# Optimization experiments

Measured on AMD Instinct MI355X. Metric: run time of the kernel, lower is better.

Reference implementation:

```python
import jax, jax.numpy as jnp
import numpy as np

B, L, D = 4, 4096, 1024
N_HEADS = 16
HEAD_SIZE = D // N_HEADS  # 64


def setup_inputs() -> dict:
    key = jax.random.key(0)
    k_x, k_w, k_m = jax.random.split(key, 3)
    x = jax.random.normal(k_x, (B, L, D), dtype=jnp.float32)
    # nn.Linear(D, 3*head_size, bias=False): weight (3*hs, D); store transposed (D, 3*hs)
    W_qkv = jax.random.normal(k_w, (D, 3 * HEAD_SIZE), dtype=jnp.float32) * (D ** -0.5)
    attn_mask = jax.random.randint(k_m, (B, L), 0, 2).astype(jnp.bool_)
    return {"x": x, "attn_mask": attn_mask, "W_qkv": W_qkv}


def reference(x, attn_mask, W_qkv):
    # x: (B, L, D); W_qkv: (D, 3*hs); attn_mask: (B, L) True = attend
    qkv = x @ W_qkv                                # (B, L, 3*hs)
    q, k, v = jnp.split(qkv, 3, axis=-1)           # each (B, L, hs)
    scale = HEAD_SIZE ** -0.5
    scores = jnp.einsum('bqd,bkd->bqk', q, k) * scale   # (B, L, L)
    neg_inf = jnp.finfo(scores.dtype).min
    scores = jnp.where(attn_mask[:, None, :], scores, neg_inf)
    weights = jax.nn.softmax(scores, axis=-1)      # (B, L, L)
    out = jnp.einsum('bqk,bkd->bqd', weights, v)   # (B, L, hs)
    return out
```

## Files before the change

kernel.cpp:

```cpp
#include <hip/hip_runtime.h>

typedef __bf16 bf16_t;
typedef __bf16 bf16x8 __attribute__((ext_vector_type(8)));
typedef __bf16 bf16x4 __attribute__((ext_vector_type(4)));
typedef __bf16 bf16x2 __attribute__((ext_vector_type(2)));
typedef float  f32x4  __attribute__((ext_vector_type(4)));
typedef float  f32x16 __attribute__((ext_vector_type(16)));
struct uint4_t { unsigned x, y, z, w; };

#define B_  4
#define L_  4096
#define D_  1024
#define HS  64
#define NQ  192
#define SCL2E 0.1803368801111204f
#define MFMA16 __builtin_amdgcn_mfma_f32_16x16x32_bf16
#define MFMA32 __builtin_amdgcn_mfma_f32_32x32x16_bf16

#if defined(__has_builtin)
# if __has_builtin(__builtin_amdgcn_global_load_lds)
#  define HAS_GLL 1
# endif
#endif
#ifndef HAS_GLL
# define HAS_GLL 0
#endif

static __device__ __forceinline__ unsigned pk_bf16(float a, float b) {
    union { bf16x2 v; unsigned u; } x;
    x.v[0] = (bf16_t)a; x.v[1] = (bf16_t)b;
    return x.u;
}
static __device__ __forceinline__ void swap32(unsigned& x, unsigned& y) {
    asm("v_permlane32_swap_b32 %0, %1" : "+v"(x), "+v"(y));
}

__global__ __launch_bounds__(256) void pack_w_kernel(const void* __restrict__ Win,
                                                     const unsigned char* __restrict__ mask,
                                                     const unsigned short* __restrict__ xw,
                                                     bf16_t* __restrict__ Wtp,
                                                     int* __restrict__ flags,
                                                     bf16_t* __restrict__ m01) {
    __shared__ int c1, c23, cbad;
    int tid = threadIdx.x;
    if (tid == 0) { c1 = 0; c23 = 0; cbad = 0; }
    __syncthreads();
    uint4_t m[4];
#pragma unroll
    for (int i = 0; i < 4; ++i)
        m[i] = *(const uint4_t*)(mask + tid * 16 + i * 4096);
    int a = 0, bc = 0;
#pragma unroll
    for (int i = 0; i < 4; ++i) {
        const unsigned* w = (const unsigned*)&m[i];
#pragma unroll
        for (int j = 0; j < 4; ++j) {
            if (w[j] & 0x0000ff00u) a++;
            if (w[j] & 0xffff0000u) bc++;
        }
    }
    uint4_t xm = *(const uint4_t*)(xw + tid * 8);
    int bad = 0;
    const unsigned* xwv = (const unsigned*)&xm;
#pragma unroll
    for (int j = 0; j < 4; ++j)
#pragma unroll
        for (int h = 0; h < 2; ++h) {
            unsigned s = (xwv[j] >> (16 * h)) & 0xFFFFu;
            unsigned e = (s >> 7) & 0xFF;
            if (e > 150 || (e < 90 && e != 0)) bad++;
        }
    if (a)   atomicAdd(&c1, a);
    if (bc)  atomicAdd(&c23, bc);
    if (bad) atomicAdd(&cbad, bad);
    __syncthreads();
    int f32 = (cbad >= 64) ? 1 : 0;
    int kind = (c1 > 0) ? 1 : ((c23 > 0) ? 2 : 0);
    if (blockIdx.x == 0 && tid == 0) {
        flags[0] = kind;
        flags[1] = f32;
    }

    int idx = blockIdx.x * 256 + tid;

    if (idx < B_ * L_) {
        bool mv;
        if (kind == 1)      mv = mask[idx] != 0;
        else if (kind == 2) mv = ((const float*)mask)[idx] != 0.0f;
        else                mv = ((const int*)mask)[idx] != 0;
        m01[idx] = (bf16_t)(mv ? 1.0f : 0.0f);
    }

    int lane = idx & 63;
    int t    = (idx >> 6) & 3;
    int kc   = (idx >> 8) & 31;
    int ct   = idx >> 13;
    int n  = ct * 64 + t * 16 + (lane & 15);
    int k0 = kc * 32 + (lane >> 4) * 8;
    bf16x8 v;
#pragma unroll
    for (int j = 0; j < 8; ++j) {
        if (f32) v[j] = (bf16_t)(((const float*)Win)[(k0 + j) * NQ + n]);
        else     v[j] = ((const bf16_t*)Win)[(k0 + j) * NQ + n];
    }
    *(bf16x8*)(Wtp + (size_t)idx * 8) = v;
}

__global__ __launch_bounds__(256, 2) void qkv_gemm_kernel(const void* __restrict__ xin,
                                                          const int* __restrict__ flags,
                                                          const bf16_t* __restrict__ Wtp,
                                                          const bf16_t* __restrict__ m01p,
                                                          bf16_t* __restrict__ Qb,
                                                          bf16_t* __restrict__ Kp,
                                                          bf16_t* __restrict__ Vp) {
    __shared__ __align__(16) bf16_t xs[32 * 520];
    __shared__ __align__(16) bf16_t sqk[32 * 136];
    __shared__ __align__(16) bf16_t sv[64 * 40];

    int tid = threadIdx.x;
    int wave = tid >> 6, lane = tid & 63, quad = lane >> 4, l16 = lane & 15;
    int rg = wave & 1, ch = wave >> 1;
    int m0 = blockIdx.x * 32;
    int xf = flags[1];

    f32x4 acc[6] = {};
    bf16x8 Ba[6], Bb[6];

    auto stage = [&](int h) {
        bf16x8 tmp[8];
#pragma unroll
        for (int j = 0; j < 8; ++j) {
            int c = tid + j * 256;
            int row = c >> 6, off = (c & 63) * 8;
            if (xf) {
                const float* xp = (const float*)xin + (size_t)(m0 + row) * D_ + h * 512 + off;
                f32x4 lo = *(const f32x4*)xp, hi = *(const f32x4*)(xp + 4);
                tmp[j][0] = (bf16_t)lo[0]; tmp[j][1] = (bf16_t)lo[1];
                tmp[j][2] = (bf16_t)lo[2]; tmp[j][3] = (bf16_t)lo[3];
                tmp[j][4] = (bf16_t)hi[0]; tmp[j][5] = (bf16_t)hi[1];
                tmp[j][6] = (bf16_t)hi[2]; tmp[j][7] = (bf16_t)hi[3];
            } else {
                tmp[j] = *(const bf16x8*)((const bf16_t*)xin + (size_t)(m0 + row) * D_ + h * 512 + off);
            }
        }
#pragma unroll
        for (int j = 0; j < 8; ++j) {
            int c = tid + j * 256;
            int row = c >> 6, off = (c & 63) * 8;
            *(bf16x8*)&xs[row * 520 + off] = tmp[j];
        }
    };
    auto loadB6 = [&](int ks, bf16x8* Bv) {
#pragma unroll
        for (int i = 0; i < 6; ++i) {
            int st = ch * 6 + i, ct2 = st >> 2, tt = st & 3;
            Bv[i] = *(const bf16x8*)(Wtp + ((size_t)(ct2 * 32 + ks) * 4 + tt) * 512 + lane * 8);
        }
    };
    auto compute6 = [&](int ks, const bf16x8* Bv) {
        bf16x8 A = *(const bf16x8*)&xs[(rg * 16 + l16) * 520 + (ks & 15) * 32 + quad * 8];
#pragma unroll
        for (int i = 0; i < 6; ++i)
            acc[i] = MFMA16(A, Bv[i], acc[i], 0, 0, 0);
    };

    stage(0);
    loadB6(0, Ba);
    __syncthreads();
#pragma unroll
    for (int half = 0; half < 2; ++half) {
        int base = half * 16;
        for (int m = 0; m < 16; m += 2) {
            int ks = base + m;
            loadB6(ks + 1, Bb);
            compute6(ks, Ba);
            loadB6(ks + 2 <= 31 ? ks + 2 : 31, Ba);
            compute6(ks + 1, Bb);
        }
        if (half == 0) {
            __syncthreads();
            stage(1);
            __syncthreads();
        }
    }

    int rowb = rg * 16 + quad * 4;
#pragma unroll
    for (int i = 0; i < 6; ++i) {
        int col = ch * 96 + i * 16 + l16;
#pragma unroll
        for (int r = 0; r < 4; ++r) {
            float av = acc[i][r];
            if (col < 64) av *= SCL2E;
            bf16_t hv = (bf16_t)av;
            if (col < 128) sqk[(rowb + r) * 136 + col] = hv;
            else           sv[(col - 128) * 40 + rowb + r] = hv;
        }
    }
    __syncthreads();

    int bb = m0 >> 12, l0 = m0 & 4095;
    int t64 = l0 >> 6, stile = (l0 >> 5) & 1, ctop = (l0 >> 4) & 2;
    {
        int row = tid >> 3, off = (tid & 7) * 8;
        bf16x8 v = *(const bf16x8*)&sqk[row * 136 + off];
        *(bf16x8*)(Qb + (size_t)(m0 + row) * HS + off) = v;
    }
    {
        int chk = tid >> 6, ln = tid & 63;
        bf16x8 v = *(const bf16x8*)&sqk[(tid & 31) * 136 + 64 + chk * 16 + ((tid >> 5) & 1) * 8];
        *(bf16x8*)(Kp + (size_t)bb * (L_ * HS) +
                   ((((size_t)t64 * 2 + stile) * 4 + chk) * 64 + ln) * 8) = v;
    }
    {
        int dt = tid >> 7, chL = (tid >> 6) & 1, ln = tid & 63;
        int hi2 = (tid >> 5) & 1, d31 = tid & 31;
        bf16x8 v  = *(const bf16x8*)&sv[(dt * 32 + d31) * 40 + chL * 16 + hi2 * 8];
        bf16x8 mm = *(const bf16x8*)(m01p + (size_t)m0 + chL * 16 + hi2 * 8);
        bf16x8 o;
#pragma unroll
        for (int j = 0; j < 8; ++j) o[j] = (bf16_t)((float)v[j] * (float)mm[j]);
        *(bf16x8*)(Vp + (size_t)bb * (L_ * HS) +
                   ((((size_t)t64 * 2 + dt) * 4 + ctop + chL) * 64 + ln) * 8) = o;
    }
}

template<int NSPLIT>
__global__ __launch_bounds__(256, 2) void attn_kernel(const bf16_t* __restrict__ Qb,
                                                      const bf16_t* __restrict__ Kp,
                                                      const bf16_t* __restrict__ Vp,
                                                      const bf16_t* __restrict__ m01p,
                                                      const int* __restrict__ flags,
                                                      float* __restrict__ Opart,
                                                      float* __restrict__ lpart,
                                                      void* __restrict__ outv) {
    constexpr int KCH = L_ / NSPLIT;
    constexpr int NHT = KCH / 32;
    __shared__ __align__(16) bf16_t ktile[4][2][2048];

    int tid = threadIdx.x, wave = tid >> 6, lane = tid & 63;
    int hi = lane >> 5, l31 = lane & 31;
    int grp = blockIdx.x % (B_ * NSPLIT);
    int qt  = blockIdx.x / (B_ * NSPLIT);
    int sp = grp / B_, b = grp % B_;
    int q0 = qt * 128 + wave * 32;
    int hb = sp * NHT;

    const bf16_t* KpB = Kp + (size_t)b * (L_ * HS);
    const bf16_t* VpB = Vp + (size_t)b * (L_ * HS);
    const bf16_t* mB  = m01p + (size_t)b * L_ + sp * KCH;

    bf16x8 Qf[4];
    {
        const bf16_t* qp = Qb + (size_t)(b * L_ + q0 + l31) * HS + hi * 8;
#pragma unroll
        for (int c = 0; c < 4; ++c) Qf[c] = *(const bf16x8*)(qp + c * 16);
    }

    f32x16 O0 = {}, O1 = {}, den = {};

    auto stage = [&](int buf, int ht) {
        const bf16_t* src = KpB + (size_t)ht * 2048;
        bf16_t* dst = &ktile[wave][buf][0];
#if HAS_GLL
#pragma unroll
        for (int j = 0; j < 4; ++j)
            __builtin_amdgcn_global_load_lds(
                (const __attribute__((address_space(1))) unsigned*)(src + (j * 64 + lane) * 8),
                (__attribute__((address_space(3))) unsigned*)(dst + (j * 64 + lane) * 8), 16, 0, 0);
#else
#pragma unroll
        for (int j = 0; j < 4; ++j)
            *(bf16x8*)(dst + (j * 64 + lane) * 8) = *(const bf16x8*)(src + (j * 64 + lane) * 8);
#endif
    };

    stage(0, hb);
    if (NHT > 1) stage(1, hb + 1);

    for (int t = 0; t < NHT; ++t) {
        int ht = hb + t;
        int t64 = ht >> 1, stile = ht & 1;
        const bf16_t* vt = VpB + (size_t)t64 * 4096;
        const bf16_t* mt = mB + t * 32;

        bf16x8 V0[2], V1[2], Mf[2];
#pragma unroll
        for (int cc = 0; cc < 2; ++cc) {
            int chk = stile * 2 + cc;
            V0[cc] = *(const bf16x8*)(vt + (size_t)(0 * 4 + chk) * 512 + lane * 8);
            V1[cc] = *(const bf16x8*)(vt + (size_t)(1 * 4 + chk) * 512 + lane * 8);
            Mf[cc] = *(const bf16x8*)(mt + cc * 16 + hi * 8);
        }

        if (t + 1 < NHT) { asm volatile("s_waitcnt vmcnt(10)" ::: "memory"); }
        else             { asm volatile("s_waitcnt vmcnt(6)"  ::: "memory"); }

        const bf16_t* kl = &ktile[wave][t & 1][0];
        bf16x8 Kfr[4];
#pragma unroll
        for (int c = 0; c < 4; ++c)
            Kfr[c] = *(const bf16x8*)(kl + c * 512 + lane * 8);
        asm volatile("s_waitcnt lgkmcnt(0)" ::: "memory");
        __builtin_amdgcn_sched_barrier(0);
        if (t + 2 < NHT) stage(t & 1, ht + 2);

        f32x16 S = {};
        __builtin_amdgcn_s_setprio(1);
#pragma unroll
        for (int c = 0; c < 4; ++c)
            S = MFMA32(Kfr[c], Qf[c], S, 0, 0, 0);
        __builtin_amdgcn_s_setprio(0);
#pragma unroll
        for (int r = 0; r < 16; ++r) S[r] = exp2f(S[r]);

#pragma unroll
        for (int cc = 0; cc < 2; ++cc) {
            unsigned w0 = pk_bf16(S[cc * 8 + 0], S[cc * 8 + 1]);
            unsigned w1 = pk_bf16(S[cc * 8 + 2], S[cc * 8 + 3]);
            unsigned w2 = pk_bf16(S[cc * 8 + 4], S[cc * 8 + 5]);
            unsigned w3 = pk_bf16(S[cc * 8 + 6], S[cc * 8 + 7]);
            swap32(w0, w2);
            swap32(w1, w3);
            union { unsigned u[4]; bf16x8 v; } P;
            P.u[0] = w0; P.u[1] = w1; P.u[2] = w2; P.u[3] = w3;
            __builtin_amdgcn_s_setprio(1);
            O0  = MFMA32(P.v, V0[cc], O0, 0, 0, 0);
            O1  = MFMA32(P.v, V1[cc], O1, 0, 0, 0);
            den = MFMA32(P.v, Mf[cc], den, 0, 0, 0);
            __builtin_amdgcn_s_setprio(0);
        }
    }

    if (NSPLIT == 1) {
        int of32 = flags[1];
#pragma unroll
        for (int r = 0; r < 16; ++r) {
            int qr = (r & 3) + 8 * (r >> 2) + 4 * hi;
            float inv = 1.0f / den[r];
            size_t base = (size_t)(b * L_ + q0 + qr) * HS;
            if (of32) {
                float* op = (float*)outv + base;
                op[l31]      = O0[r] * inv;
                op[32 + l31] = O1[r] * inv;
            } else {
                bf16_t* op = (bf16_t*)outv + base;
                op[l31]      = (bf16_t)(O0[r] * inv);
                op[32 + l31] = (bf16_t)(O1[r] * inv);
            }
        }
    } else {
        float* op = Opart + (size_t)sp * (B_ * L_ * HS) + (size_t)(b * L_ + q0) * HS + l31;
#pragma unroll
        for (int r = 0; r < 16; ++r) {
            int qr = (r & 3) + 8 * (r >> 2) + 4 * hi;
            op[(size_t)qr * HS]      = O0[r];
            op[(size_t)qr * HS + 32] = O1[r];
        }
        if (l31 == 0) {
            float* lp = lpart + (size_t)sp * (B_ * L_) + b * L_ + q0;
#pragma unroll
            for (int r = 0; r < 16; ++r)
                lp[(r & 3) + 8 * (r >> 2) + 4 * hi] = den[r];
        }
    }
}

__global__ __launch_bounds__(256) void reduce_kernel(const float* __restrict__ Opart,
                                                     const float* __restrict__ lpart,
                                                     const int* __restrict__ flags,
                                                     void* __restrict__ outv,
                                                     int nsplit) {
    int i4 = (blockIdx.x * 256 + threadIdx.x) * 4;
    int row = i4 >> 6;
    f32x4 acc = {};
    float lsum = 0.f;
    for (int s = 0; s < nsplit; ++s) {
        acc  += *(const f32x4*)&Opart[(size_t)s * (B_ * L_ * HS) + i4];
        lsum += lpart[(size_t)s * (B_ * L_) + row];
    }
    float inv = 1.0f / lsum;
    if (flags[1]) {
        f32x4 r = { acc[0] * inv, acc[1] * inv, acc[2] * inv, acc[3] * inv };
        *(f32x4*)&((float*)outv)[i4] = r;
    } else {
        bf16x4 r;
#pragma unroll
        for (int j = 0; j < 4; ++j) r[j] = (bf16_t)(acc[j] * inv);
        *(bf16x4*)&((bf16_t*)outv)[i4] = r;
    }
}

extern "C" void kernel_launch(void* const* d_in, const int* in_sizes, int n_in,
                              void* d_out, int out_size, void* d_ws, size_t ws_size,
                              hipStream_t stream) {
    (void)in_sizes; (void)n_in; (void)out_size;
    const void* x    = d_in[0];
    const void* mask = d_in[1];
    const void* W    = d_in[2];

    char* ws = (char*)d_ws;
    bf16_t* Qb    = (bf16_t*)(ws);
    bf16_t* Kp    = (bf16_t*)(ws + (2u << 20));
    bf16_t* Vp    = (bf16_t*)(ws + (4u << 20));
    bf16_t* Wtp   = (bf16_t*)(ws + (6u << 20));
    int*    flags = (int*)   (ws + (6u << 20) + (512u << 10));
    bf16_t* m01p  = (bf16_t*)(ws + (6u << 20) + (516u << 10));
    float*  Opart = (float*) (ws + (7u << 20));

    auto need = [](int ns) -> size_t {
        return (7u << 20) + (size_t)ns * (B_ * L_ * HS * 4)
                          + (size_t)ns * (B_ * L_ * 4) + 4096;
    };
    int nsplit = (ws_size >= need(8)) ? 8 : (ws_size >= need(4)) ? 4 : 1;
    float* lpart = (float*)(ws + (7u << 20) + (size_t)nsplit * (B_ * L_ * HS * 4));

    pack_w_kernel<<<96, 256, 0, stream>>>(W, (const unsigned char*)mask,
                                          (const unsigned short*)x, Wtp, flags, m01p);
    qkv_gemm_kernel<<<512, 256, 0, stream>>>(x, flags, Wtp, m01p, Qb, Kp, Vp);
    if (nsplit == 8) {
        attn_kernel<8><<<32 * B_ * 8, 256, 0, stream>>>(Qb, Kp, Vp, m01p, flags,
                                                        Opart, lpart, d_out);
        reduce_kernel<<<(B_ * L_ * HS) / 1024, 256, 0, stream>>>(Opart, lpart, flags,
                                                                 d_out, 8);
    } else if (nsplit == 4) {
        attn_kernel<4><<<32 * B_ * 4, 256, 0, stream>>>(Qb, Kp, Vp, m01p, flags,
                                                        Opart, lpart, d_out);
        reduce_kernel<<<(B_ * L_ * HS) / 1024, 256, 0, stream>>>(Opart, lpart, flags,
                                                                 d_out, 4);
    } else {
        attn_kernel<1><<<32 * B_, 256, 0, stream>>>(Qb, Kp, Vp, m01p, flags,
                                                    Opart, lpart, d_out);
    }
}
```

Before: 164.3 us.

## Load K fragments directly from global and raise key-split count to 16

Drops the per-wave LDS double-buffered staging of K tiles (global_load_lds plus waitcnt choreography) and has each lane read its K fragments straight from global memory into registers. It also raises the key-dimension split from 8 to 16 when the workspace allows, launching twice as many attention blocks and reducing over 16 partials. The aim is to remove LDS traffic and sync overhead and to expose more parallelism. The cost is that K-load latency is no longer prefetched two tiles ahead, and the partial-output writes and reduction work grow.

```diff
diff --git a/kernel.cpp b/kernel.cpp
--- a/kernel.cpp
+++ b/kernel.cpp
@@ -16,15 +16,6 @@
 #define SCL2E 0.1803368801111204f
 #define MFMA16 __builtin_amdgcn_mfma_f32_16x16x32_bf16
 #define MFMA32 __builtin_amdgcn_mfma_f32_32x32x16_bf16
-
-#if defined(__has_builtin)
-# if __has_builtin(__builtin_amdgcn_global_load_lds)
-#  define HAS_GLL 1
-# endif
-#endif
-#ifndef HAS_GLL
-# define HAS_GLL 0
-#endif
 
 static __device__ __forceinline__ unsigned pk_bf16(float a, float b) {
     union { bf16x2 v; unsigned u; } x;
@@ -236,7 +227,6 @@
                                                       void* __restrict__ outv) {
     constexpr int KCH = L_ / NSPLIT;
     constexpr int NHT = KCH / 32;
-    __shared__ __align__(16) bf16_t ktile[4][2][2048];
 
     int tid = threadIdx.x, wave = tid >> 6, lane = tid & 63;
     int hi = lane >> 5, l31 = lane & 31;
@@ -259,31 +249,17 @@
 
     f32x16 O0 = {}, O1 = {}, den = {};
 
-    auto stage = [&](int buf, int ht) {
-        const bf16_t* src = KpB + (size_t)ht * 2048;
-        bf16_t* dst = &ktile[wave][buf][0];
-#if HAS_GLL
-#pragma unroll
-        for (int j = 0; j < 4; ++j)
-            __builtin_amdgcn_global_load_lds(
-                (const __attribute__((address_space(1))) unsigned*)(src + (j * 64 + lane) * 8),
-                (__attribute__((address_space(3))) unsigned*)(dst + (j * 64 + lane) * 8), 16, 0, 0);
-#else
-#pragma unroll
-        for (int j = 0; j < 4; ++j)
-            *(bf16x8*)(dst + (j * 64 + lane) * 8) = *(const bf16x8*)(src + (j * 64 + lane) * 8);
-#endif
-    };
-
-    stage(0, hb);
-    if (NHT > 1) stage(1, hb + 1);
-
     for (int t = 0; t < NHT; ++t) {
         int ht = hb + t;
         int t64 = ht >> 1, stile = ht & 1;
+        const bf16_t* kt = KpB + (size_t)ht * 2048;
         const bf16_t* vt = VpB + (size_t)t64 * 4096;
         const bf16_t* mt = mB + t * 32;
 
+        bf16x8 Kfr[4];
+#pragma unroll
+        for (int c = 0; c < 4; ++c)
+            Kfr[c] = *(const bf16x8*)(kt + ((size_t)c * 64 + lane) * 8);
         bf16x8 V0[2], V1[2], Mf[2];
 #pragma unroll
         for (int cc = 0; cc < 2; ++cc) {
@@ -292,18 +268,6 @@
             V1[cc] = *(const bf16x8*)(vt + (size_t)(1 * 4 + chk) * 512 + lane * 8);
             Mf[cc] = *(const bf16x8*)(mt + cc * 16 + hi * 8);
         }
-
-        if (t + 1 < NHT) { asm volatile("s_waitcnt vmcnt(10)" ::: "memory"); }
-        else             { asm volatile("s_waitcnt vmcnt(6)"  ::: "memory"); }
-
-        const bf16_t* kl = &ktile[wave][t & 1][0];
-        bf16x8 Kfr[4];
-#pragma unroll
-        for (int c = 0; c < 4; ++c)
-            Kfr[c] = *(const bf16x8*)(kl + c * 512 + lane * 8);
-        asm volatile("s_waitcnt lgkmcnt(0)" ::: "memory");
-        __builtin_amdgcn_sched_barrier(0);
-        if (t + 2 < NHT) stage(t & 1, ht + 2);
 
         f32x16 S = {};
         __builtin_amdgcn_s_setprio(1);
@@ -412,22 +376,22 @@
         return (7u << 20) + (size_t)ns * (B_ * L_ * HS * 4)
                           + (size_t)ns * (B_ * L_ * 4) + 4096;
     };
-    int nsplit = (ws_size >= need(8)) ? 8 : (ws_size >= need(4)) ? 4 : 1;
+    int nsplit = (ws_size >= need(16)) ? 16 : (ws_size >= need(8)) ? 8 : 1;
     float* lpart = (float*)(ws + (7u << 20) + (size_t)nsplit * (B_ * L_ * HS * 4));
 
     pack_w_kernel<<<96, 256, 0, stream>>>(W, (const unsigned char*)mask,
                                           (const unsigned short*)x, Wtp, flags, m01p);
     qkv_gemm_kernel<<<512, 256, 0, stream>>>(x, flags, Wtp, m01p, Qb, Kp, Vp);
-    if (nsplit == 8) {
+    if (nsplit == 16) {
+        attn_kernel<16><<<32 * B_ * 16, 256, 0, stream>>>(Qb, Kp, Vp, m01p, flags,
+                                                          Opart, lpart, d_out);
+        reduce_kernel<<<(B_ * L_ * HS) / 1024, 256, 0, stream>>>(Opart, lpart, flags,
+                                                                 d_out, 16);
+    } else if (nsplit == 8) {
         attn_kernel<8><<<32 * B_ * 8, 256, 0, stream>>>(Qb, Kp, Vp, m01p, flags,
                                                         Opart, lpart, d_out);
         reduce_kernel<<<(B_ * L_ * HS) / 1024, 256, 0, stream>>>(Opart, lpart, flags,
                                                                  d_out, 8);
-    } else if (nsplit == 4) {
-        attn_kernel<4><<<32 * B_ * 4, 256, 0, stream>>>(Qb, Kp, Vp, m01p, flags,
-                                                        Opart, lpart, d_out);
-        reduce_kernel<<<(B_ * L_ * HS) / 1024, 256, 0, stream>>>(Opart, lpart, flags,
-                                                                 d_out, 4);
     } else {
         attn_kernel<1><<<32 * B_, 256, 0, stream>>>(Qb, Kp, Vp, m01p, flags,
                                                     Opart, lpart, d_out);
```

Result: no change. 164.1 us (-0.2%).
